# Kernel tuning notes

Hardware: AMD Instinct MI355X
Metric: run time of the kernel (lower is better)

## Reference

```python
import jax, jax.numpy as jnp
import numpy as np

N_NODES = 50000
N_EDGES = 500000
D = 128
BN_EPS = 1e-5


def setup_inputs() -> dict:
    key = jax.random.key(0)
    ks = jax.random.split(key, 6)
    x = jax.random.normal(ks[0], (N_NODES, D), dtype=jnp.float32)
    edge_attr = jax.random.normal(ks[1], (N_EDGES, D), dtype=jnp.float32)
    edge_source = jax.random.randint(ks[2], (N_EDGES,), 0, N_NODES, dtype=jnp.int32)
    edge_target = jax.random.randint(ks[3], (N_EDGES,), 0, N_NODES, dtype=jnp.int32)
    # Linear weights stored as [in, out] = [3*D, D]; scaled like torch default init
    scale = 1.0 / np.sqrt(3 * D)
    Wf = jax.random.normal(ks[4], (3 * D, D), dtype=jnp.float32) * scale
    Ws = jax.random.normal(ks[5], (3 * D, D), dtype=jnp.float32) * scale
    bf = jnp.zeros((D,), dtype=jnp.float32)
    bs = jnp.zeros((D,), dtype=jnp.float32)
    gamma = jnp.ones((D,), dtype=jnp.float32)
    beta = jnp.zeros((D,), dtype=jnp.float32)
    return {"x": x, "edge_attr": edge_attr, "edge_source": edge_source,
            "edge_target": edge_target, "Wf": Wf, "bf": bf, "Ws": Ws, "bs": bs,
            "gamma": gamma, "beta": beta}


def reference(x, edge_attr, edge_source, edge_target, Wf, bf, Ws, bs, gamma, beta):
    # gather + concat: z is [E, 3*D]
    z = jnp.concatenate([x[edge_source], x[edge_target], edge_attr], axis=-1)
    # gated edge messages: sigmoid(linear_f(z)) * softplus(linear_s(z))  [E, D]
    msg = jax.nn.sigmoid(z @ Wf + bf) * jax.nn.softplus(z @ Ws + bs)
    # scatter-sum back to source nodes  [N, D]
    agg = jax.ops.segment_sum(msg, edge_source, num_segments=N_NODES)
    # BatchNorm1d (training mode: batch stats, biased variance)
    mean = jnp.mean(agg, axis=0)
    var = jnp.var(agg, axis=0)
    agg_bn = (agg - mean) * jax.lax.rsqrt(var + BN_EPS) * gamma + beta
    return jax.nn.softplus(x + agg_bn)
```

## Files before the change

### kernel.cpp

```cpp
#include <hip/hip_runtime.h>
#include <math.h>
#include <stdint.h>

#define N_NODES 50000
#define N_EDGES 500000
#define D 128
#define BE 64
#define NKT 6
#define WROW 72
#define WSLAB (256 * WROW)
#define MROW 136
#define LOG2E 1.4426950408889634f
#define LN2   0.6931471805599453f

typedef __attribute__((ext_vector_type(8))) short bf16x8;
typedef __attribute__((ext_vector_type(4))) float floatx4;

__device__ __forceinline__ float fast_sigmoid(float v) {
    return __builtin_amdgcn_rcpf(1.0f + __builtin_amdgcn_exp2f(-v * LOG2E));
}
__device__ __forceinline__ float fast_softplus(float v) {
    float t = __builtin_amdgcn_exp2f(-fabsf(v) * LOG2E);
    return fmaxf(v, 0.0f) + __builtin_amdgcn_logf(1.0f + t) * LN2;
}
__device__ __forceinline__ uint32_t pack_bf16(float a, float b) {
    union { float f; uint32_t u; } ca, cb; ca.f = a; cb.f = b;
    return __builtin_amdgcn_perm(cb.u + 0x8000u, ca.u + 0x8000u, 0x07060302);
}
__device__ __forceinline__ unsigned short f2bf(float f) {
    union { float f; uint32_t u; } c; c.f = f;
    return (unsigned short)((c.u + 0x8000u) >> 16);
}

__global__ __launch_bounds__(256) void wt_prepass(
    const float* __restrict__ Wf, const float* __restrict__ Ws,
    unsigned short* __restrict__ Wt)
{
    const int kt = blockIdx.x >> 3;
    const int i  = blockIdx.x & 7;
    const int n  = threadIdx.x;
    const float* src = (n < 128) ? (Wf + n) : (Ws + (n - 128));
    const int k0 = kt * 64 + i * 8;
    uint32_t u[4];
#pragma unroll
    for (int j = 0; j < 4; j++) {
        float a = src[(size_t)(k0 + 2 * j) * D];
        float b = src[(size_t)(k0 + 2 * j + 1) * D];
        u[j] = pack_bf16(a, b);
    }
    uint4 v; v.x = u[0]; v.y = u[1]; v.z = u[2]; v.w = u[3];
    *(uint4*)(Wt + (size_t)(kt * 256 + n) * WROW + i * 8) = v;
}

__global__ __launch_bounds__(256) void edge_msg_mfma(
    const float* __restrict__ x, const float* __restrict__ edge_attr,
    const int* __restrict__ esrc, const int* __restrict__ etgt,
    const unsigned short* __restrict__ Wt,
    const float* __restrict__ bfp, const float* __restrict__ bsp,
    float* __restrict__ agg, unsigned short* __restrict__ msgs,
    int* __restrict__ cnt, int mode)
{
    __shared__ unsigned short sW[WSLAB];
    __shared__ unsigned short sZ[BE * WROW];
    __shared__ int sSrc[BE];
    __shared__ int sTgt[BE];

    const int tid  = threadIdx.x;
    const int lane = tid & 63;
    const int w    = tid >> 6;
    const int e0   = blockIdx.x * BE;

    if (tid < BE) {
        sSrc[tid] = (e0 + tid < N_EDGES) ? esrc[e0 + tid] : 0;
    } else if (tid < 2 * BE) {
        int m = tid - BE;
        sTgt[m] = (e0 + m < N_EDGES) ? etgt[e0 + m] : 0;
    }
    __syncthreads();

    floatx4 acc[4][4];
#pragma unroll
    for (int mt = 0; mt < 4; mt++)
#pragma unroll
        for (int nt = 0; nt < 4; nt++) {
            floatx4 z = {0.f, 0.f, 0.f, 0.f};
            acc[mt][nt] = z;
        }

    const int zm = tid >> 2;
    const int zk = (tid & 3) * 16;

#pragma unroll 1
    for (int kt = 0; kt < NKT; kt++) {
        {
            const char* gbase = (const char*)Wt + (size_t)kt * 36864 + w * 9216 + lane * 16;
            char* lbase = (char*)sW + w * 9216;
#pragma unroll
            for (int i = 0; i < 9; i++) {
                __builtin_amdgcn_global_load_lds(
                    (const __attribute__((address_space(1))) void*)(gbase + i * 1024),
                    (__attribute__((address_space(3))) void*)(lbase + i * 1024),
                    16, 0, 0);
            }
        }
        {
            const float* zsrc;
            int half = (kt & 1) * 64;
            if (kt < 2)      zsrc = x + (size_t)sSrc[zm] * D + half;
            else if (kt < 4) zsrc = x + (size_t)sTgt[zm] * D + half;
            else {
                int eg = e0 + zm;
                zsrc = edge_attr + (size_t)(eg < N_EDGES ? eg : 0) * D + half;
            }
            float4 f0 = *(const float4*)(zsrc + zk);
            float4 f1 = *(const float4*)(zsrc + zk + 4);
            float4 f2 = *(const float4*)(zsrc + zk + 8);
            float4 f3 = *(const float4*)(zsrc + zk + 12);
            uint4 lo, hi;
            lo.x = pack_bf16(f0.x, f0.y); lo.y = pack_bf16(f0.z, f0.w);
            lo.z = pack_bf16(f1.x, f1.y); lo.w = pack_bf16(f1.z, f1.w);
            hi.x = pack_bf16(f2.x, f2.y); hi.y = pack_bf16(f2.z, f2.w);
            hi.z = pack_bf16(f3.x, f3.y); hi.w = pack_bf16(f3.z, f3.w);
            uint32_t* dz = (uint32_t*)(sZ + (size_t)zm * WROW) + (zk >> 1);
            *(uint4*)(dz)     = lo;
            *(uint4*)(dz + 4) = hi;
        }
        __syncthreads();

#pragma unroll
        for (int ks = 0; ks < 2; ks++) {
            const int kb = ks * 32 + (lane >> 4) * 8;
            bf16x8 afr[4];
#pragma unroll
            for (int mt = 0; mt < 4; mt++)
                afr[mt] = *(const bf16x8*)(sZ + (mt * 16 + (lane & 15)) * WROW + kb);
            bf16x8 bfr[4];
#pragma unroll
            for (int nt = 0; nt < 4; nt++) {
                int n = (nt < 2) ? (w * 32 + nt * 16 + (lane & 15))
                                 : (128 + w * 32 + (nt - 2) * 16 + (lane & 15));
                bfr[nt] = *(const bf16x8*)(sW + n * WROW + kb);
            }
#pragma unroll
            for (int mt = 0; mt < 4; mt++)
#pragma unroll
                for (int nt = 0; nt < 4; nt++)
                    acc[mt][nt] = __builtin_amdgcn_mfma_f32_16x16x32_bf16(
                        afr[mt], bfr[nt], acc[mt][nt], 0, 0, 0);
        }
        __syncthreads();
    }

    if (mode) {
        unsigned short* sM = sW;
#pragma unroll
        for (int nt = 0; nt < 2; nt++) {
            const int col = w * 32 + nt * 16 + (lane & 15);
            const float bF = bfp[col];
            const float bS = bsp[col];
#pragma unroll
            for (int mt = 0; mt < 4; mt++) {
#pragma unroll
                for (int r = 0; r < 4; r++) {
                    int mm = mt * 16 + (lane >> 4) * 4 + r;
                    float f = acc[mt][nt][r] + bF;
                    float s = acc[mt][nt + 2][r] + bS;
                    sM[mm * MROW + col] = f2bf(fast_sigmoid(f) * fast_softplus(s));
                }
            }
        }
        __syncthreads();
        {
            const int r = tid >> 2;
            const int c = tid & 3;
            if (e0 + r < N_EDGES) {
                const uint4* sp = (const uint4*)(sM + r * MROW + c * 32);
                uint4 v0 = sp[0], v1 = sp[1], v2 = sp[2], v3 = sp[3];
                uint4* dp = (uint4*)(msgs + (size_t)(e0 + r) * D + c * 32);
                dp[0] = v0; dp[1] = v1; dp[2] = v2; dp[3] = v3;
            }
        }
        if (tid < BE && e0 + tid < N_EDGES) atomicAdd(&cnt[sSrc[tid]], 1);
    } else {
#pragma unroll
        for (int nt = 0; nt < 2; nt++) {
            const int col = w * 32 + nt * 16 + (lane & 15);
            const float bF = bfp[col];
            const float bS = bsp[col];
#pragma unroll
            for (int mt = 0; mt < 4; mt++) {
#pragma unroll
                for (int r = 0; r < 4; r++) {
                    int mm = mt * 16 + (lane >> 4) * 4 + r;
                    int eg = e0 + mm;
                    if (eg >= N_EDGES) continue;
                    float f = acc[mt][nt][r] + bF;
                    float s = acc[mt][nt + 2][r] + bS;
                    atomicAdd(agg + (size_t)sSrc[mm] * D + col,
                              fast_sigmoid(f) * fast_softplus(s));
                }
            }
        }
    }
}

__global__ __launch_bounds__(1024) void scan1_kernel(
    const int* __restrict__ cnt, int* __restrict__ ofs, int* __restrict__ bsum)
{
    __shared__ int sh[1024];
    const int t = threadIdx.x;
    const int n = blockIdx.x * 1024 + t;
    int c = (n < N_NODES) ? cnt[n] : 0;
    sh[t] = c;
    __syncthreads();
    for (int off = 1; off < 1024; off <<= 1) {
        int v = (t >= off) ? sh[t - off] : 0;
        __syncthreads();
        sh[t] += v;
        __syncthreads();
    }
    if (n < N_NODES) ofs[n] = sh[t] - c;
    if (t == 1023) bsum[blockIdx.x] = sh[1023];
}

__global__ __launch_bounds__(64) void scan2_kernel(int* __restrict__ bsum)
{
    if (threadIdx.x == 0) {
        int v[49];
#pragma unroll
        for (int i = 0; i < 49; i++) v[i] = bsum[i];
        int run = 0;
#pragma unroll
        for (int i = 0; i < 49; i++) { bsum[i] = run; run += v[i]; }
    }
}

__global__ __launch_bounds__(512) void fill_kernel(
    const int* __restrict__ esrc, int* __restrict__ ofs,
    const int* __restrict__ bsum, int* __restrict__ eidx)
{
    int e = blockIdx.x * 512 + threadIdx.x;
    if (e < N_EDGES) {
        int s = esrc[e];
        int slot = atomicAdd(&ofs[s], 1) + bsum[s >> 10];
        eidx[slot] = e;
    }
}

__global__ __launch_bounds__(256) void gather_kernel(
    const unsigned short* __restrict__ msgs, const int* __restrict__ eidx,
    const int* __restrict__ cnt, const int* __restrict__ ofs,
    const int* __restrict__ bsum, float* __restrict__ agg)
{
    __shared__ float red[2][64][2];
    const int tid  = threadIdx.x;
    const int lane = tid & 63;
    const int w2   = (tid >> 6) & 1;
    const int h    = tid >> 7;
    const int n    = blockIdx.x * 2 + h;
    const int deg  = cnt[n];
    const int base = bsum[n >> 10] + ofs[n] - deg;
    float a0 = 0.0f, a1 = 0.0f;
    for (int j = w2; j < deg; j += 2) {
        int id = eidx[base + j];
        uint32_t p = *(const uint32_t*)(msgs + (size_t)id * D + 2 * lane);
        union { uint32_t u; float f; } c0, c1;
        c0.u = p << 16;
        c1.u = p & 0xFFFF0000u;
        a0 += c0.f; a1 += c1.f;
    }
    if (w2 == 1) { red[h][lane][0] = a0; red[h][lane][1] = a1; }
    __syncthreads();
    if (w2 == 0) {
        a0 += red[h][lane][0];
        a1 += red[h][lane][1];
        float2 o; o.x = a0; o.y = a1;
        *(float2*)(agg + (size_t)n * D + 2 * lane) = o;
    }
}

#define STATS_BLOCKS 128
__global__ __launch_bounds__(256) void bn_stats_kernel(
    const float* __restrict__ agg, float* __restrict__ stats)
{
    __shared__ float4 redS[256];
    __shared__ float4 redQ[256];
    const int c4 = threadIdx.x & 31;
    const int rg = threadIdx.x >> 5;
    const int rows = (N_NODES + STATS_BLOCKS - 1) / STATS_BLOCKS;
    const int r0 = blockIdx.x * rows;
    const int r1 = min(r0 + rows, N_NODES);
    const float4* a4 = (const float4*)agg;

    float4 s = {0, 0, 0, 0}, q = {0, 0, 0, 0};
    for (int r = r0 + rg; r < r1; r += 8) {
        float4 v = a4[(size_t)r * 32 + c4];
        s.x += v.x; s.y += v.y; s.z += v.z; s.w += v.w;
        q.x += v.x * v.x; q.y += v.y * v.y; q.z += v.z * v.z; q.w += v.w * v.w;
    }
    redS[threadIdx.x] = s;
    redQ[threadIdx.x] = q;
    __syncthreads();
    if (rg == 0) {
#pragma unroll
        for (int j = 1; j < 8; j++) {
            float4 ts = redS[c4 + j * 32], tq = redQ[c4 + j * 32];
            s.x += ts.x; s.y += ts.y; s.z += ts.z; s.w += ts.w;
            q.x += tq.x; q.y += tq.y; q.z += tq.z; q.w += tq.w;
        }
        atomicAdd(&stats[c4 * 4 + 0], s.x);
        atomicAdd(&stats[c4 * 4 + 1], s.y);
        atomicAdd(&stats[c4 * 4 + 2], s.z);
        atomicAdd(&stats[c4 * 4 + 3], s.w);
        atomicAdd(&stats[D + c4 * 4 + 0], q.x);
        atomicAdd(&stats[D + c4 * 4 + 1], q.y);
        atomicAdd(&stats[D + c4 * 4 + 2], q.z);
        atomicAdd(&stats[D + c4 * 4 + 3], q.w);
    }
}

__global__ __launch_bounds__(256) void bn_final_kernel(
    const float* __restrict__ x, const float* __restrict__ agg,
    const float* __restrict__ stats,
    const float* __restrict__ gamma, const float* __restrict__ beta,
    float* __restrict__ out)
{
    const int idx = blockIdx.x * blockDim.x + threadIdx.x;
    const int total4 = N_NODES * D / 4;
    if (idx >= total4) return;
    const int c4 = idx & (D / 4 - 1);
    const float inv_n = 1.0f / (float)N_NODES;

    float4 sm = *(const float4*)&stats[c4 * 4];
    float4 sq = *(const float4*)&stats[D + c4 * 4];
    float4 g  = *(const float4*)&gamma[c4 * 4];
    float4 b  = *(const float4*)&beta[c4 * 4];
    float4 xv = ((const float4*)x)[idx];
    float4 av = ((const float4*)agg)[idx];

    float4 o;
    {
        float mean = sm.x * inv_n, var = sq.x * inv_n - mean * mean;
        float is = rsqrtf(var + 1e-5f) * g.x;
        o.x = fast_softplus(xv.x + (av.x - mean) * is + b.x);
    }
    {
        float mean = sm.y * inv_n, var = sq.y * inv_n - mean * mean;
        float is = rsqrtf(var + 1e-5f) * g.y;
        o.y = fast_softplus(xv.y + (av.y - mean) * is + b.y);
    }
    {
        float mean = sm.z * inv_n, var = sq.z * inv_n - mean * mean;
        float is = rsqrtf(var + 1e-5f) * g.z;
        o.z = fast_softplus(xv.z + (av.z - mean) * is + b.z);
    }
    {
        float mean = sm.w * inv_n, var = sq.w * inv_n - mean * mean;
        float is = rsqrtf(var + 1e-5f) * g.w;
        o.w = fast_softplus(xv.w + (av.w - mean) * is + b.w);
    }
    ((float4*)out)[idx] = o;
}

extern "C" void kernel_launch(void* const* d_in, const int* in_sizes, int n_in,
                              void* d_out, int out_size, void* d_ws, size_t ws_size,
                              hipStream_t stream) {
    const float* x         = (const float*)d_in[0];
    const float* edge_attr = (const float*)d_in[1];
    const int*   esrc      = (const int*)d_in[2];
    const int*   etgt      = (const int*)d_in[3];
    const float* Wf        = (const float*)d_in[4];
    const float* bf_       = (const float*)d_in[5];
    const float* Ws        = (const float*)d_in[6];
    const float* bs_       = (const float*)d_in[7];
    const float* gamma     = (const float*)d_in[8];
    const float* beta      = (const float*)d_in[9];
    float* out = (float*)d_out;

    float* agg   = (float*)d_ws;
    float* stats = agg + (size_t)N_NODES * D;
    int*   cnt   = (int*)(stats + 2 * D);
    int*   ofs   = cnt + N_NODES;
    int*   bsum  = ofs + N_NODES;
    unsigned short* Wt = (unsigned short*)(bsum + 256);
    int*   eidx  = (int*)((char*)Wt + 221184);
    unsigned short* msgs = (unsigned short*)(eidx + N_EDGES);
    const size_t NEED = 25600000ULL + 1024 + 200000 + 200000 + 1024
                      + 221184 + 2000000 + 128000000ULL;
    const int mode = (ws_size >= NEED) ? 1 : 0;

    wt_prepass<<<48, 256, 0, stream>>>(Wf, Ws, Wt);
    if (mode) {
        hipMemsetAsync(stats, 0, 1024 + 200000, stream);
        edge_msg_mfma<<<(N_EDGES + BE - 1) / BE, 256, 0, stream>>>(
            x, edge_attr, esrc, etgt, Wt, bf_, bs_, agg, msgs, cnt, 1);
        scan1_kernel<<<49, 1024, 0, stream>>>(cnt, ofs, bsum);
        scan2_kernel<<<1, 64, 0, stream>>>(bsum);
        fill_kernel<<<(N_EDGES + 511) / 512, 512, 0, stream>>>(esrc, ofs, bsum, eidx);
        gather_kernel<<<N_NODES / 2, 256, 0, stream>>>(msgs, eidx, cnt, ofs, bsum, agg);
    } else {
        hipMemsetAsync(d_ws, 0, ((size_t)N_NODES * D + 2 * D) * sizeof(float), stream);
        edge_msg_mfma<<<(N_EDGES + BE - 1) / BE, 256, 0, stream>>>(
            x, edge_attr, esrc, etgt, Wt, bf_, bs_, agg, msgs, cnt, 0);
    }
    bn_stats_kernel<<<STATS_BLOCKS, 256, 0, stream>>>(agg, stats);
    bn_final_kernel<<<(N_NODES * D / 4 + 255) / 256, 256, 0, stream>>>(
        x, agg, stats, gamma, beta, out);
}
```

Measured before the change: 661.6 us.

## Double edge tile to 128 and read weights directly from global

```diff
diff --git a/kernel.cpp b/kernel.cpp
--- a/kernel.cpp
+++ b/kernel.cpp
@@ -5,10 +5,8 @@
 #define N_NODES 50000
 #define N_EDGES 500000
 #define D 128
-#define BE 64
-#define NKT 6
+#define BE 128
 #define WROW 72
-#define WSLAB (256 * WROW)
 #define MROW 136
 #define LOG2E 1.4426950408889634f
 #define LN2   0.6931471805599453f
@@ -52,7 +50,7 @@
     *(uint4*)(Wt + (size_t)(kt * 256 + n) * WROW + i * 8) = v;
 }
 
-__global__ __launch_bounds__(256) void edge_msg_mfma(
+__global__ __launch_bounds__(256, 2) void edge_msg_mfma(
     const float* __restrict__ x, const float* __restrict__ edge_attr,
     const int* __restrict__ esrc, const int* __restrict__ etgt,
     const unsigned short* __restrict__ Wt,
@@ -60,8 +58,7 @@
     float* __restrict__ agg, unsigned short* __restrict__ msgs,
     int* __restrict__ cnt, int mode)
 {
-    __shared__ unsigned short sW[WSLAB];
-    __shared__ unsigned short sZ[BE * WROW];
+    __shared__ unsigned short sZ[BE * MROW];
     __shared__ int sSrc[BE];
     __shared__ int sTgt[BE];
 
@@ -72,97 +69,93 @@
 
     if (tid < BE) {
         sSrc[tid] = (e0 + tid < N_EDGES) ? esrc[e0 + tid] : 0;
-    } else if (tid < 2 * BE) {
+    } else {
         int m = tid - BE;
         sTgt[m] = (e0 + m < N_EDGES) ? etgt[e0 + m] : 0;
     }
     __syncthreads();
 
-    floatx4 acc[4][4];
-#pragma unroll
-    for (int mt = 0; mt < 4; mt++)
+    floatx4 acc[8][4];
+#pragma unroll
+    for (int mt = 0; mt < 8; mt++)
 #pragma unroll
         for (int nt = 0; nt < 4; nt++) {
             floatx4 z = {0.f, 0.f, 0.f, 0.f};
             acc[mt][nt] = z;
         }
 
-    const int zm = tid >> 2;
-    const int zk = (tid & 3) * 16;
-
 #pragma unroll 1
-    for (int kt = 0; kt < NKT; kt++) {
+    for (int kp = 0; kp < 3; kp++) {
         {
-            const char* gbase = (const char*)Wt + (size_t)kt * 36864 + w * 9216 + lane * 16;
-            char* lbase = (char*)sW + w * 9216;
-#pragma unroll
-            for (int i = 0; i < 9; i++) {
-                __builtin_amdgcn_global_load_lds(
-                    (const __attribute__((address_space(1))) void*)(gbase + i * 1024),
-                    (__attribute__((address_space(3))) void*)(lbase + i * 1024),
-                    16, 0, 0);
-            }
-        }
-        {
-            const float* zsrc;
-            int half = (kt & 1) * 64;
-            if (kt < 2)      zsrc = x + (size_t)sSrc[zm] * D + half;
-            else if (kt < 4) zsrc = x + (size_t)sTgt[zm] * D + half;
+            const int row = tid >> 1;
+            const int hf  = tid & 1;
+            const float* src;
+            if (kp == 0)      src = x + (size_t)sSrc[row] * D;
+            else if (kp == 1) src = x + (size_t)sTgt[row] * D;
             else {
-                int eg = e0 + zm;
-                zsrc = edge_attr + (size_t)(eg < N_EDGES ? eg : 0) * D + half;
-            }
-            float4 f0 = *(const float4*)(zsrc + zk);
-            float4 f1 = *(const float4*)(zsrc + zk + 4);
-            float4 f2 = *(const float4*)(zsrc + zk + 8);
-            float4 f3 = *(const float4*)(zsrc + zk + 12);
-            uint4 lo, hi;
-            lo.x = pack_bf16(f0.x, f0.y); lo.y = pack_bf16(f0.z, f0.w);
-            lo.z = pack_bf16(f1.x, f1.y); lo.w = pack_bf16(f1.z, f1.w);
-            hi.x = pack_bf16(f2.x, f2.y); hi.y = pack_bf16(f2.z, f2.w);
-            hi.z = pack_bf16(f3.x, f3.y); hi.w = pack_bf16(f3.z, f3.w);
-            uint32_t* dz = (uint32_t*)(sZ + (size_t)zm * WROW) + (zk >> 1);
-            *(uint4*)(dz)     = lo;
-            *(uint4*)(dz + 4) = hi;
+                int eg = e0 + row;
+                src = edge_attr + (size_t)(eg < N_EDGES ? eg : 0) * D;
+            }
+            src += hf * 64;
+            uint32_t* dz = (uint32_t*)(sZ + row * MROW + hf * 64);
+#pragma unroll
+            for (int g = 0; g < 4; g++) {
+                float4 a  = *(const float4*)(src + g * 16);
+                float4 b  = *(const float4*)(src + g * 16 + 4);
+                float4 cc = *(const float4*)(src + g * 16 + 8);
+                float4 dd = *(const float4*)(src + g * 16 + 12);
+                uint4 u, v;
+                u.x = pack_bf16(a.x, a.y);   u.y = pack_bf16(a.z, a.w);
+                u.z = pack_bf16(b.x, b.y);   u.w = pack_bf16(b.z, b.w);
+                v.x = pack_bf16(cc.x, cc.y); v.y = pack_bf16(cc.z, cc.w);
+                v.z = pack_bf16(dd.x, dd.y); v.w = pack_bf16(dd.z, dd.w);
+                *(uint4*)(dz + g * 8)     = u;
+                *(uint4*)(dz + g * 8 + 4) = v;
+            }
         }
         __syncthreads();
 
 #pragma unroll
-        for (int ks = 0; ks < 2; ks++) {
-            const int kb = ks * 32 + (lane >> 4) * 8;
-            bf16x8 afr[4];
-#pragma unroll
-            for (int mt = 0; mt < 4; mt++)
-                afr[mt] = *(const bf16x8*)(sZ + (mt * 16 + (lane & 15)) * WROW + kb);
-            bf16x8 bfr[4];
-#pragma unroll
-            for (int nt = 0; nt < 4; nt++) {
-                int n = (nt < 2) ? (w * 32 + nt * 16 + (lane & 15))
-                                 : (128 + w * 32 + (nt - 2) * 16 + (lane & 15));
-                bfr[nt] = *(const bf16x8*)(sW + n * WROW + kb);
-            }
-#pragma unroll
-            for (int mt = 0; mt < 4; mt++)
-#pragma unroll
-                for (int nt = 0; nt < 4; nt++)
-                    acc[mt][nt] = __builtin_amdgcn_mfma_f32_16x16x32_bf16(
-                        afr[mt], bfr[nt], acc[mt][nt], 0, 0, 0);
+        for (int kh = 0; kh < 2; kh++) {
+            const int kt = kp * 2 + kh;
+            const unsigned short* wb = Wt + (size_t)kt * 256 * WROW;
+#pragma unroll
+            for (int ks = 0; ks < 2; ks++) {
+                const int kb = ks * 32 + ((lane >> 4) << 3);
+                bf16x8 bfr[4];
+#pragma unroll
+                for (int nt = 0; nt < 4; nt++) {
+                    const int n = ((nt < 2) ? (w * 32 + nt * 16)
+                                            : (128 + w * 32 + (nt - 2) * 16))
+                                  + (lane & 15);
+                    bfr[nt] = *(const bf16x8*)(wb + n * WROW + kb);
+                }
+#pragma unroll
+                for (int mt = 0; mt < 8; mt++) {
+                    bf16x8 afr = *(const bf16x8*)(sZ + (mt * 16 + (lane & 15)) * MROW
+                                                  + kh * 64 + kb);
+#pragma unroll
+                    for (int nt = 0; nt < 4; nt++)
+                        acc[mt][nt] = __builtin_amdgcn_mfma_f32_16x16x32_bf16(
+                            afr, bfr[nt], acc[mt][nt], 0, 0, 0);
+                }
+            }
         }
         __syncthreads();
     }
 
     if (mode) {
-        unsigned short* sM = sW;
+        unsigned short* sM = sZ;
 #pragma unroll
         for (int nt = 0; nt < 2; nt++) {
             const int col = w * 32 + nt * 16 + (lane & 15);
             const float bF = bfp[col];
             const float bS = bsp[col];
 #pragma unroll
-            for (int mt = 0; mt < 4; mt++) {
+            for (int mt = 0; mt < 8; mt++) {
 #pragma unroll
                 for (int r = 0; r < 4; r++) {
-                    int mm = mt * 16 + (lane >> 4) * 4 + r;
+                    int mm = mt * 16 + ((lane >> 4) << 2) + r;
                     float f = acc[mt][nt][r] + bF;
                     float s = acc[mt][nt + 2][r] + bS;
                     sM[mm * MROW + col] = f2bf(fast_sigmoid(f) * fast_softplus(s));
@@ -171,13 +164,15 @@
         }
         __syncthreads();
         {
-            const int r = tid >> 2;
-            const int c = tid & 3;
+            const int r = tid >> 1;
+            const int c = tid & 1;
             if (e0 + r < N_EDGES) {
-                const uint4* sp = (const uint4*)(sM + r * MROW + c * 32);
+                const uint4* sp = (const uint4*)(sM + r * MROW + c * 64);
+                uint4* dp = (uint4*)(msgs + (size_t)(e0 + r) * D + c * 64);
                 uint4 v0 = sp[0], v1 = sp[1], v2 = sp[2], v3 = sp[3];
-                uint4* dp = (uint4*)(msgs + (size_t)(e0 + r) * D + c * 32);
+                uint4 v4 = sp[4], v5 = sp[5], v6 = sp[6], v7 = sp[7];
                 dp[0] = v0; dp[1] = v1; dp[2] = v2; dp[3] = v3;
+                dp[4] = v4; dp[5] = v5; dp[6] = v6; dp[7] = v7;
             }
         }
         if (tid < BE && e0 + tid < N_EDGES) atomicAdd(&cnt[sSrc[tid]], 1);
@@ -188,10 +183,10 @@
             const float bF = bfp[col];
             const float bS = bsp[col];
 #pragma unroll
-            for (int mt = 0; mt < 4; mt++) {
+            for (int mt = 0; mt < 8; mt++) {
 #pragma unroll
                 for (int r = 0; r < 4; r++) {
-                    int mm = mt * 16 + (lane >> 4) * 4 + r;
+                    int mm = mt * 16 + ((lane >> 4) << 2) + r;
                     int eg = e0 + mm;
                     if (eg >= N_EDGES) continue;
                     float f = acc[mt][nt][r] + bF;
```

Result: slower. 685.4 us (+3.6%).

## Double edge tile to 128 with 8 waves sharing each weight slab

Applied to the files above, without the earlier changes.

```diff
diff --git a/kernel.cpp b/kernel.cpp
--- a/kernel.cpp
+++ b/kernel.cpp
@@ -5,10 +5,9 @@
 #define N_NODES 50000
 #define N_EDGES 500000
 #define D 128
-#define BE 64
+#define BE 128
 #define NKT 6
 #define WROW 72
-#define WSLAB (256 * WROW)
 #define MROW 136
 #define LOG2E 1.4426950408889634f
 #define LN2   0.6931471805599453f
@@ -52,7 +51,7 @@
     *(uint4*)(Wt + (size_t)(kt * 256 + n) * WROW + i * 8) = v;
 }
 
-__global__ __launch_bounds__(256) void edge_msg_mfma(
+__global__ __launch_bounds__(512, 4) void edge_msg_mfma(
     const float* __restrict__ x, const float* __restrict__ edge_attr,
     const int* __restrict__ esrc, const int* __restrict__ etgt,
     const unsigned short* __restrict__ Wt,
@@ -60,7 +59,7 @@
     float* __restrict__ agg, unsigned short* __restrict__ msgs,
     int* __restrict__ cnt, int mode)
 {
-    __shared__ unsigned short sW[WSLAB];
+    __shared__ unsigned short sW[256 * WROW];
     __shared__ unsigned short sZ[BE * WROW];
     __shared__ int sSrc[BE];
     __shared__ int sTgt[BE];
@@ -68,6 +67,8 @@
     const int tid  = threadIdx.x;
     const int lane = tid & 63;
     const int w    = tid >> 6;
+    const int wc   = w & 3;
+    const int wr   = w >> 2;
     const int e0   = blockIdx.x * BE;
 
     if (tid < BE) {
@@ -93,14 +94,17 @@
 #pragma unroll 1
     for (int kt = 0; kt < NKT; kt++) {
         {
-            const char* gbase = (const char*)Wt + (size_t)kt * 36864 + w * 9216 + lane * 16;
-            char* lbase = (char*)sW + w * 9216;
-#pragma unroll
-            for (int i = 0; i < 9; i++) {
-                __builtin_amdgcn_global_load_lds(
-                    (const __attribute__((address_space(1))) void*)(gbase + i * 1024),
-                    (__attribute__((address_space(3))) void*)(lbase + i * 1024),
-                    16, 0, 0);
+            const char* gbase = (const char*)Wt + (size_t)kt * 36864 + lane * 16;
+            char* lbase = (char*)sW;
+#pragma unroll
+            for (int i = 0; i < 5; i++) {
+                int c = w + i * 8;
+                if (c < 36) {
+                    __builtin_amdgcn_global_load_lds(
+                        (const __attribute__((address_space(1))) void*)(gbase + c * 1024),
+                        (__attribute__((address_space(3))) void*)(lbase + c * 1024),
+                        16, 0, 0);
+                }
             }
         }
         {
@@ -133,12 +137,12 @@
             bf16x8 afr[4];
 #pragma unroll
             for (int mt = 0; mt < 4; mt++)
-                afr[mt] = *(const bf16x8*)(sZ + (mt * 16 + (lane & 15)) * WROW + kb);
+                afr[mt] = *(const bf16x8*)(sZ + (wr * 64 + mt * 16 + (lane & 15)) * WROW + kb);
             bf16x8 bfr[4];
 #pragma unroll
             for (int nt = 0; nt < 4; nt++) {
-                int n = (nt < 2) ? (w * 32 + nt * 16 + (lane & 15))
-                                 : (128 + w * 32 + (nt - 2) * 16 + (lane & 15));
+                int n = (nt < 2) ? (wc * 32 + nt * 16 + (lane & 15))
+                                 : (128 + wc * 32 + (nt - 2) * 16 + (lane & 15));
                 bfr[nt] = *(const bf16x8*)(sW + n * WROW + kb);
             }
 #pragma unroll
@@ -155,14 +159,14 @@
         unsigned short* sM = sW;
 #pragma unroll
         for (int nt = 0; nt < 2; nt++) {
-            const int col = w * 32 + nt * 16 + (lane & 15);
+            const int col = wc * 32 + nt * 16 + (lane & 15);
             const float bF = bfp[col];
             const float bS = bsp[col];
 #pragma unroll
             for (int mt = 0; mt < 4; mt++) {
 #pragma unroll
                 for (int r = 0; r < 4; r++) {
-                    int mm = mt * 16 + (lane >> 4) * 4 + r;
+                    int mm = wr * 64 + mt * 16 + (lane >> 4) * 4 + r;
                     float f = acc[mt][nt][r] + bF;
                     float s = acc[mt][nt + 2][r] + bS;
                     sM[mm * MROW + col] = f2bf(fast_sigmoid(f) * fast_softplus(s));
@@ -184,14 +188,14 @@
     } else {
 #pragma unroll
         for (int nt = 0; nt < 2; nt++) {
-            const int col = w * 32 + nt * 16 + (lane & 15);
+            const int col = wc * 32 + nt * 16 + (lane & 15);
             const float bF = bfp[col];
             const float bS = bsp[col];
 #pragma unroll
             for (int mt = 0; mt < 4; mt++) {
 #pragma unroll
                 for (int r = 0; r < 4; r++) {
-                    int mm = mt * 16 + (lane >> 4) * 4 + r;
+                    int mm = wr * 64 + mt * 16 + (lane >> 4) * 4 + r;
                     int eg = e0 + mm;
                     if (eg >= N_EDGES) continue;
                     float f = acc[mt][nt][r] + bF;
@@ -392,7 +396,7 @@
     wt_prepass<<<48, 256, 0, stream>>>(Wf, Ws, Wt);
     if (mode) {
         hipMemsetAsync(stats, 0, 1024 + 200000, stream);
-        edge_msg_mfma<<<(N_EDGES + BE - 1) / BE, 256, 0, stream>>>(
+        edge_msg_mfma<<<(N_EDGES + BE - 1) / BE, 512, 0, stream>>>(
             x, edge_attr, esrc, etgt, Wt, bf_, bs_, agg, msgs, cnt, 1);
         scan1_kernel<<<49, 1024, 0, stream>>>(cnt, ofs, bsum);
         scan2_kernel<<<1, 64, 0, stream>>>(bsum);
@@ -400,7 +404,7 @@
         gather_kernel<<<N_NODES / 2, 256, 0, stream>>>(msgs, eidx, cnt, ofs, bsum, agg);
     } else {
         hipMemsetAsync(d_ws, 0, ((size_t)N_NODES * D + 2 * D) * sizeof(float), stream);
-        edge_msg_mfma<<<(N_EDGES + BE - 1) / BE, 256, 0, stream>>>(
+        edge_msg_mfma<<<(N_EDGES + BE - 1) / BE, 512, 0, stream>>>(
             x, edge_attr, esrc, etgt, Wt, bf_, bs_, agg, msgs, cnt, 0);
     }
     bn_stats_kernel<<<STATS_BLOCKS, 256, 0, stream>>>(agg, stats);
```

Result: no change. 649.2 us (-1.9%).
